# Kernel optimization log

Measured on AMD Instinct MI355X. Metric: run time of the kernel, lower is better.

The kernel has to match this reference:

```python
import jax, jax.numpy as jnp
import numpy as np

N = 100000
E = 1000000
IN_C, HID, OUT_C = 128, 128, 40
DROPOUT_P = 0.5
BN_EPS = 1e-5


def setup_inputs() -> dict:
    key = jax.random.key(0)
    ks = jax.random.split(key, 10)
    x = jax.random.normal(ks[0], (N, IN_C), dtype=jnp.float32)
    edge_index = jax.random.randint(ks[1], (2, E), 0, N, dtype=jnp.int32)

    def glorot(k, fan_in, fan_out):
        lim = np.sqrt(6.0 / (fan_in + fan_out)).astype(np.float32)
        return jax.random.uniform(k, (fan_in, fan_out), jnp.float32, -lim, lim)

    return {
        "x": x,
        "edge_index": edge_index,
        "W1": glorot(ks[2], IN_C, HID), "b1": jnp.zeros((HID,), jnp.float32),
        "g1": jnp.ones((HID,), jnp.float32), "be1": jnp.zeros((HID,), jnp.float32),
        "W2": glorot(ks[3], HID, HID), "b2": jnp.zeros((HID,), jnp.float32),
        "g2": jnp.ones((HID,), jnp.float32), "be2": jnp.zeros((HID,), jnp.float32),
        "W3": glorot(ks[4], HID, OUT_C), "b3": jnp.zeros((OUT_C,), jnp.float32),
    }


def _deg_inv_sqrt(dst):
    # degree from destination nodes, +1 for the added self loop (PyG gcn_norm)
    deg = jax.ops.segment_sum(jnp.ones((E,), jnp.float32), dst, num_segments=N) + 1.0
    return jax.lax.rsqrt(deg)


def _gcn_conv(h, W, b, src, dst, dinv):
    # h: [N, Cin] -> [N, Cout]; y = D^-1/2 (A + I) D^-1/2 (h W) + b
    hw = h @ W
    norm = dinv[src] * dinv[dst]                      # [E]
    msg = hw[src] * norm[:, None]                     # [E, Cout] gather (memory-bound)
    agg = jax.ops.segment_sum(msg, dst, num_segments=N)
    agg = agg + hw * (dinv * dinv)[:, None]           # self-loop contribution
    return agg + b


def _batchnorm(h, gamma, beta):
    mu = jnp.mean(h, axis=0)
    var = jnp.mean(jnp.square(h - mu), axis=0)        # biased, training mode
    return (h - mu) * jax.lax.rsqrt(var + BN_EPS) * gamma + beta


def _dropout(h, key):
    keep = jax.random.bernoulli(key, 1.0 - DROPOUT_P, h.shape)
    return jnp.where(keep, h / (1.0 - DROPOUT_P), 0.0)


def reference(x, edge_index, W1, b1, g1, be1, W2, b2, g2, be2, W3, b3):
    src, dst = edge_index[0], edge_index[1]
    dinv = _deg_inv_sqrt(dst)
    dk = jax.random.split(jax.random.key(42), 2)

    h = _gcn_conv(x, W1, b1, src, dst, dinv)
    h = _dropout(jax.nn.relu(_batchnorm(h, g1, be1)), dk[0])

    h = _gcn_conv(h, W2, b2, src, dst, dinv)
    h = _dropout(jax.nn.relu(_batchnorm(h, g2, be2)), dk[1])

    h = _gcn_conv(h, W3, b3, src, dst, dinv)
    return jax.nn.log_softmax(h, axis=1)
```

## Files before the change

### kernel.cpp

```cpp
#include <hip/hip_runtime.h>
#include <math.h>

typedef __attribute__((ext_vector_type(8))) short bf16x8;
typedef __attribute__((ext_vector_type(4))) float f32x4;

__device__ __forceinline__ float bfbits2f(unsigned short b){
  return __uint_as_float(((unsigned)b) << 16);
}
__device__ __forceinline__ unsigned short f2bfbits(float f){
  unsigned u = __float_as_uint(f);
  unsigned r = u + 0x7fffu + ((u >> 16) & 1u);
  return (unsigned short)(r >> 16);
}

__device__ __forceinline__ uint4 ld16(const void* __restrict__ base, unsigned byteoff){
  return *(const uint4*)((const char*)base + byteoff);
}
__device__ __forceinline__ uint2 ld8(const void* __restrict__ base, unsigned byteoff){
  return *(const uint2*)((const char*)base + byteoff);
}

__host__ __device__ __forceinline__ unsigned rotl32(unsigned v, int d){
  return (v << d) | (v >> (32 - d));
}
__host__ __device__ __forceinline__ void tf2x32(unsigned k0, unsigned k1,
                                                unsigned c0, unsigned c1,
                                                unsigned &o0, unsigned &o1)
{
  unsigned ks2 = k0 ^ k1 ^ 0x1BD11BDAu;
  unsigned x0 = c0 + k0, x1 = c1 + k1;
#define TFR(r) x0 += x1; x1 = rotl32(x1, r); x1 ^= x0;
  TFR(13) TFR(15) TFR(26) TFR(6)
  x0 += k1;  x1 += ks2 + 1u;
  TFR(17) TFR(29) TFR(16) TFR(24)
  x0 += ks2; x1 += k0 + 2u;
  TFR(13) TFR(15) TFR(26) TFR(6)
  x0 += k0;  x1 += k1 + 3u;
  TFR(17) TFR(29) TFR(16) TFR(24)
  x0 += k1;  x1 += ks2 + 4u;
  TFR(13) TFR(15) TFR(26) TFR(6)
  x0 += ks2; x1 += k0 + 5u;
#undef TFR
  o0 = x0; o1 = x1;
}

__global__ __launch_bounds__(256) void k_init(const float* __restrict__ W1,
                                              const float* __restrict__ W2,
                                              const float* __restrict__ W3,
                                              unsigned short* __restrict__ WT1,
                                              unsigned short* __restrict__ WT2,
                                              unsigned short* __restrict__ WT3,
                                              uint4* __restrict__ zbase, int zwords)
{
  if (blockIdx.x < 3){
    const float* W; unsigned short* WT; int Cout, Cpad;
    if (blockIdx.x == 0){ W = W1; WT = WT1; Cout = 128; Cpad = 128; }
    else if (blockIdx.x == 1){ W = W2; WT = WT2; Cout = 128; Cpad = 128; }
    else { W = W3; WT = WT3; Cout = 40; Cpad = 48; }
    int tot = Cpad * 128;
    for (int i = threadIdx.x; i < tot; i += 256){
      int n = i >> 7, k = i & 127;
      float v = (n < Cout) ? W[k * Cout + n] : 0.f;
      WT[i] = f2bfbits(v);
    }
  } else {
    int idx = (blockIdx.x - 3) * 256 + threadIdx.x;
    if (idx < zwords) zbase[idx] = make_uint4(0u, 0u, 0u, 0u);
  }
}

__global__ __launch_bounds__(256) void k_countpos(const int* __restrict__ dst,
                                                  int* __restrict__ cnt,
                                                  int* __restrict__ pos, int E)
{
  int g = blockIdx.x * 256 + threadIdx.x;
  int base = g * 4;
  if (base + 3 < E){
    int4 d = ((const int4*)dst)[g];
    int4 p;
    p.x = atomicAdd(&cnt[d.x], 1);
    p.y = atomicAdd(&cnt[d.y], 1);
    p.z = atomicAdd(&cnt[d.z], 1);
    p.w = atomicAdd(&cnt[d.w], 1);
    ((int4*)pos)[g] = p;
  } else {
    for (int j = 0; j < 4; j++){
      int e = base + j;
      if (e < E) pos[e] = atomicAdd(&cnt[dst[e]], 1);
    }
  }
}

__global__ __launch_bounds__(256) void k_blocksum(const int* __restrict__ cnt,
                                                  int* __restrict__ bsum, int N)
{
  __shared__ int sh[256];
  int t = threadIdx.x;
  int base = blockIdx.x * 1024 + t * 4;
  int s = 0;
  #pragma unroll
  for (int j = 0; j < 4; j++){ int i = base + j; if (i < N) s += cnt[i]; }
  sh[t] = s; __syncthreads();
  for (int off = 128; off; off >>= 1){
    if (t < off) sh[t] += sh[t + off];
    __syncthreads();
  }
  if (t == 0) bsum[blockIdx.x] = sh[0];
}

__global__ __launch_bounds__(256) void k_scanfinal(const int* __restrict__ cnt,
                                                   const int* __restrict__ bsum,
                                                   int* __restrict__ rowstart,
                                                   float* __restrict__ dinv,
                                                   int NB, int N)
{
  __shared__ int sh[256];
  int t = threadIdx.x;
  int vb = (t < NB) ? bsum[t] : 0;
  sh[t] = vb; __syncthreads();
  for (int off = 1; off < 256; off <<= 1){
    int x = sh[t];
    int y = (t >= off) ? sh[t - off] : 0;
    __syncthreads();
    sh[t] = x + y;
    __syncthreads();
  }
  if (blockIdx.x == 0 && t == 0) rowstart[N] = sh[NB - 1];
  int boffb = sh[blockIdx.x] - bsum[blockIdx.x];
  __syncthreads();
  int base = blockIdx.x * 1024 + t * 4;
  int c0 = 0, c1 = 0, c2 = 0, c3 = 0;
  if (base + 0 < N) c0 = cnt[base + 0];
  if (base + 1 < N) c1 = cnt[base + 1];
  if (base + 2 < N) c2 = cnt[base + 2];
  if (base + 3 < N) c3 = cnt[base + 3];
  int s = c0 + c1 + c2 + c3;
  sh[t] = s; __syncthreads();
  for (int off = 1; off < 256; off <<= 1){
    int x = sh[t];
    int y = (t >= off) ? sh[t - off] : 0;
    __syncthreads();
    sh[t] = x + y;
    __syncthreads();
  }
  int excl = sh[t] - s + boffb;
  if (base + 0 < N){ rowstart[base+0] = excl;          dinv[base+0] = rsqrtf((float)c0 + 1.f); }
  if (base + 1 < N){ rowstart[base+1] = excl+c0;       dinv[base+1] = rsqrtf((float)c1 + 1.f); }
  if (base + 2 < N){ rowstart[base+2] = excl+c0+c1;    dinv[base+2] = rsqrtf((float)c2 + 1.f); }
  if (base + 3 < N){ rowstart[base+3] = excl+c0+c1+c2; dinv[base+3] = rsqrtf((float)c3 + 1.f); }
}

__device__ __forceinline__ void fill_body(int bid,
                                          const int* __restrict__ src,
                                          const int* __restrict__ dst,
                                          const int* __restrict__ pos,
                                          const int* __restrict__ rowstart,
                                          int* __restrict__ csr, int E)
{
  int g = bid * 256 + threadIdx.x;
  int base = g * 4;
  if (base + 3 < E){
    int4 d = ((const int4*)dst)[g];
    int4 p = ((const int4*)pos)[g];
    int4 s = ((const int4*)src)[g];
    int r0 = rowstart[d.x], r1 = rowstart[d.y], r2 = rowstart[d.z], r3 = rowstart[d.w];
    csr[r0 + p.x] = s.x;
    csr[r1 + p.y] = s.y;
    csr[r2 + p.z] = s.z;
    csr[r3 + p.w] = s.w;
  } else {
    for (int j = 0; j < 4; j++){
      int e = base + j;
      if (e < E) csr[rowstart[dst[e]] + pos[e]] = src[e];
    }
  }
}

template<int NT, int MODE, int MASKGEN>
__device__ __forceinline__ void gemm_body(int bid,
                                          const void* __restrict__ Ap,
                                          const unsigned short* __restrict__ WT,
                                          const float* __restrict__ dinv,
                                          const float* __restrict__ stats,
                                          const float* __restrict__ g,
                                          const float* __restrict__ be,
                                          const unsigned* __restrict__ mask,
                                          unsigned* __restrict__ maskw,
                                          unsigned wk0, unsigned wk1, int Mw,
                                          float invN,
                                          unsigned short* __restrict__ outb,
                                          int N, int Cstride)
{
  __shared__ uint4 Wl4[NT * 16 * 16];
  __shared__ float bnS[128], bnB[128];
  const int t = threadIdx.x;
  const int w = t >> 6, l = t & 63;
  const int lm = l & 15, q = l >> 4;
  const long rb0 = (long)bid * 64;
  const int wrow0 = w * 16;
  const long grow = rb0 + wrow0 + lm;
  const bool inr = (grow < N);

  uint4 rawU[4];
  float4 rawF[4][2];
  uint4 mws;
  if (inr){
    #pragma unroll
    for (int kt = 0; kt < 4; kt++){
      int c = kt * 4 + q;
      if (MODE == 0){
        const float* ap = (const float*)Ap + grow * 128 + c * 8;
        rawF[kt][0] = *(const float4*)ap;
        rawF[kt][1] = *(const float4*)(ap + 4);
      } else {
        rawU[kt] = *(const uint4*)((const unsigned short*)Ap + grow * 128 + c * 8);
      }
    }
    if (MODE == 2) mws = *(const uint4*)(mask + ((unsigned)grow << 2));
  }

  {
    const uint4* s4 = (const uint4*)WT;
    const int tot = NT * 16 * 16;
    for (int i = t; i < tot; i += 256){
      int n = i >> 4, c = i & 15;
      Wl4[n * 16 + (c ^ (n & 15))] = s4[i];
    }
  }
  if (MODE == 2 && t < 128){
    float ss = 0.f, qq = 0.f;
    #pragma unroll
    for (int i = 0; i < 16; i++){
      ss += stats[i * 256 + t];
      qq += stats[i * 256 + 128 + t];
    }
    float mean = ss * invN;
    float var = fmaxf(qq * invN - mean * mean, 0.f);
    float rstd = rsqrtf(var + 1e-5f);
    float sc = g[t] * rstd;
    bnS[t] = sc * 2.f;
    bnB[t] = (be[t] - mean * sc) * 2.f;
  }
  __syncthreads();

  bf16x8 afr[4];
  #pragma unroll
  for (int kt = 0; kt < 4; kt++){
    uint4 chunk = make_uint4(0u, 0u, 0u, 0u);
    if (inr){
      if (MODE == 0){
        chunk.x = (unsigned)f2bfbits(rawF[kt][0].x) | ((unsigned)f2bfbits(rawF[kt][0].y) << 16);
        chunk.y = (unsigned)f2bfbits(rawF[kt][0].z) | ((unsigned)f2bfbits(rawF[kt][0].w) << 16);
        chunk.z = (unsigned)f2bfbits(rawF[kt][1].x) | ((unsigned)f2bfbits(rawF[kt][1].y) << 16);
        chunk.w = (unsigned)f2bfbits(rawF[kt][1].z) | ((unsigned)f2bfbits(rawF[kt][1].w) << 16);
      } else {
        int c = kt * 4 + q;
        unsigned mb = (&mws.x)[kt] >> (q * 8);
        const unsigned* rw = &rawU[kt].x;
        unsigned* cw = &chunk.x;
        #pragma unroll
        for (int h = 0; h < 4; h++){
          int ch = c * 8 + 2 * h;
          float f0 = bfbits2f((unsigned short)(rw[h] & 0xffffu));
          float f1 = bfbits2f((unsigned short)(rw[h] >> 16));
          f0 = fmaxf(fmaf(f0, bnS[ch],     bnB[ch]),     0.f);
          f1 = fmaxf(fmaf(f1, bnS[ch + 1], bnB[ch + 1]), 0.f);
          f0 = ((mb >> (2 * h))     & 1u) ? 0.f : f0;
          f1 = ((mb >> (2 * h + 1)) & 1u) ? 0.f : f1;
          cw[h] = (unsigned)f2bfbits(f0) | ((unsigned)f2bfbits(f1) << 16);
        }
      }
    }
    afr[kt] = *(bf16x8*)&chunk;
  }

  f32x4 acc[NT];
  #pragma unroll
  for (int nt = 0; nt < NT; nt++){
    acc[nt][0] = 0.f; acc[nt][1] = 0.f; acc[nt][2] = 0.f; acc[nt][3] = 0.f;
  }

  #pragma unroll
  for (int kt = 0; kt < 4; kt++){
    const int x = kt * 4 + q;
    #pragma unroll
    for (int nt = 0; nt < NT; nt++){
      int brow = nt * 16 + lm;
      bf16x8 wf = *(const bf16x8*)&Wl4[brow * 16 + (x ^ (brow & 15))];
      acc[nt] = __builtin_amdgcn_mfma_f32_16x16x32_bf16(wf, afr[kt], acc[nt], 0, 0, 0);
    }
  }

  if (inr){
    float dv = dinv[grow];
    char* rowp = (char*)outb + (size_t)grow * (unsigned)Cstride * 2u + (unsigned)(q * 4) * 2u;
    #pragma unroll
    for (int nt = 0; nt < NT; nt++){
      uint2 o;
      o.x = (unsigned)f2bfbits(acc[nt][0] * dv) | ((unsigned)f2bfbits(acc[nt][1] * dv) << 16);
      o.y = (unsigned)f2bfbits(acc[nt][2] * dv) | ((unsigned)f2bfbits(acc[nt][3] * dv) << 16);
      *(uint2*)(rowp + nt * 32) = o;
    }
  }

  if (MASKGEN){
    int gg = bid * 256 + t;
    if (gg < Mw){
      unsigned bits = 0u;
      #pragma unroll 4
      for (int j = 0; j < 32; j++){
        unsigned w0, w1;
        tf2x32(wk0, wk1, 0u, (unsigned)gg * 32u + (unsigned)j, w0, w1);
        bits |= (((w0 ^ w1) >> 31) << j);
      }
      maskw[gg] = bits;
    }
  }
}

__global__ __launch_bounds__(256) void k_g1f(const void* __restrict__ Ap,
                                             const unsigned short* __restrict__ WT,
                                             const float* __restrict__ dinv,
                                             unsigned* __restrict__ maskw,
                                             unsigned wk0, unsigned wk1, int Mw,
                                             unsigned short* __restrict__ outb, int N,
                                             const int* __restrict__ src,
                                             const int* __restrict__ dst,
                                             const int* __restrict__ pos,
                                             const int* __restrict__ rowstart,
                                             int* __restrict__ csr, int E, int gg)
{
  if ((int)blockIdx.x < gg){
    gemm_body<8, 0, 1>(blockIdx.x, Ap, WT, dinv, nullptr, nullptr, nullptr,
                       nullptr, maskw, wk0, wk1, Mw, 0.f, outb, N, 128);
  } else {
    fill_body(blockIdx.x - gg, src, dst, pos, rowstart, csr, E);
  }
}

template<int NT, int MODE, int MASKGEN>
__global__ __launch_bounds__(256) void k_gemm_mfma(const void* __restrict__ Ap,
                                                   const unsigned short* __restrict__ WT,
                                                   const float* __restrict__ dinv,
                                                   const float* __restrict__ stats,
                                                   const float* __restrict__ g,
                                                   const float* __restrict__ be,
                                                   const unsigned* __restrict__ mask,
                                                   unsigned* __restrict__ maskw,
                                                   unsigned wk0, unsigned wk1, int Mw,
                                                   float invN,
                                                   unsigned short* __restrict__ outb,
                                                   int N, int Cstride)
{
  gemm_body<NT, MODE, MASKGEN>(blockIdx.x, Ap, WT, dinv, stats, g, be, mask,
                               maskw, wk0, wk1, Mw, invN, outb, N, Cstride);
}

#define ACC8(U) do{ uint4 _u = (U); \
  a0 += __uint_as_float(_u.x << 16); \
  a1 += __uint_as_float(_u.x & 0xffff0000u); \
  a2 += __uint_as_float(_u.y << 16); \
  a3 += __uint_as_float(_u.y & 0xffff0000u); \
  a4 += __uint_as_float(_u.z << 16); \
  a5 += __uint_as_float(_u.z & 0xffff0000u); \
  a6 += __uint_as_float(_u.w << 16); \
  a7 += __uint_as_float(_u.w & 0xffff0000u); }while(0)

__global__ __launch_bounds__(256) void k_agg128s(const unsigned short* __restrict__ hw,
                                                 const int* __restrict__ rs,
                                                 const int* __restrict__ csr,
                                                 const float* __restrict__ dinv,
                                                 unsigned short* __restrict__ outb,
                                                 float* __restrict__ stats,
                                                 int N)
{
  const int l = threadIdx.x;
  const int ns = l >> 4;
  const int sl = l & 15;
  const int ty = threadIdx.y;
  const int grp = ty * 4 + ns;
  const int base = blockIdx.x * 32;
  const unsigned slB = (unsigned)sl * 16u;

  float s0=0.f,s1=0.f,s2=0.f,s3=0.f,s4=0.f,s5=0.f,s6=0.f,s7=0.f;
  float q0=0.f,q1=0.f,q2=0.f,q3=0.f,q4=0.f,q5=0.f,q6=0.f,q7=0.f;

  #pragma unroll 1
  for (int it = 0; it < 2; it++){
    int v = base + it * 16 + grp;
    if (v < N){
      float a0=0.f,a1=0.f,a2=0.f,a3=0.f,a4=0.f,a5=0.f,a6=0.f,a7=0.f;
      ACC8(ld16(hw, (unsigned)v * 256u + slB));
      int e0 = rs[v], e1 = rs[v + 1];
      int i = e0;
      for (; i + 4 <= e1; i += 4){
        int sa = csr[i], sb = csr[i+1], sc = csr[i+2], sd = csr[i+3];
        uint4 m0 = ld16(hw, (unsigned)sa * 256u + slB);
        uint4 m1 = ld16(hw, (unsigned)sb * 256u + slB);
        uint4 m2 = ld16(hw, (unsigned)sc * 256u + slB);
        uint4 m3 = ld16(hw, (unsigned)sd * 256u + slB);
        ACC8(m0); ACC8(m1); ACC8(m2); ACC8(m3);
      }
      for (; i < e1; i++){
        ACC8(ld16(hw, (unsigned)csr[i] * 256u + slB));
      }
      float dv = dinv[v];
      a0*=dv; a1*=dv; a2*=dv; a3*=dv; a4*=dv; a5*=dv; a6*=dv; a7*=dv;
      uint4 o;
      o.x = (unsigned)f2bfbits(a0) | ((unsigned)f2bfbits(a1) << 16);
      o.y = (unsigned)f2bfbits(a2) | ((unsigned)f2bfbits(a3) << 16);
      o.z = (unsigned)f2bfbits(a4) | ((unsigned)f2bfbits(a5) << 16);
      o.w = (unsigned)f2bfbits(a6) | ((unsigned)f2bfbits(a7) << 16);
      *(uint4*)((char*)outb + (unsigned)v * 256u + slB) = o;
      s0+=a0; q0=fmaf(a0,a0,q0);  s1+=a1; q1=fmaf(a1,a1,q1);
      s2+=a2; q2=fmaf(a2,a2,q2);  s3+=a3; q3=fmaf(a3,a3,q3);
      s4+=a4; q4=fmaf(a4,a4,q4);  s5+=a5; q5=fmaf(a5,a5,q5);
      s6+=a6; q6=fmaf(a6,a6,q6);  s7+=a7; q7=fmaf(a7,a7,q7);
    }
  }

  __shared__ float shS[16][128], shQ[16][128];
  *(float4*)&shS[grp][sl * 8]     = make_float4(s0, s1, s2, s3);
  *(float4*)&shS[grp][sl * 8 + 4] = make_float4(s4, s5, s6, s7);
  *(float4*)&shQ[grp][sl * 8]     = make_float4(q0, q1, q2, q3);
  *(float4*)&shQ[grp][sl * 8 + 4] = make_float4(q4, q5, q6, q7);
  __syncthreads();
  int t = ty * 64 + threadIdx.x;
  if (t < 128){
    float ss = 0.f, qq = 0.f;
    #pragma unroll
    for (int g2 = 0; g2 < 16; g2++){ ss += shS[g2][t]; qq += shQ[g2][t]; }
    float* dstat = stats + (blockIdx.x & 15) * 256;
    atomicAdd(&dstat[t], ss);
    atomicAdd(&dstat[128 + t], qq);
  }
}

__global__ __launch_bounds__(256) void k_agg40lsm(const unsigned short* __restrict__ hw,
                                                  const int* __restrict__ rs,
                                                  const int* __restrict__ csr,
                                                  const float* __restrict__ dinv,
                                                  const float* __restrict__ b3,
                                                  float* __restrict__ out, int N)
{
  const int l = threadIdx.x;
  const int ns = l >> 4, sl = l & 15;
  const int v = blockIdx.x * 16 + threadIdx.y * 4 + ns;
  const bool act = (v < N) && (sl < 10);
  const unsigned slB = (unsigned)sl * 8u;
  float a0 = 0.f, a1 = 0.f, a2 = 0.f, a3 = 0.f, dv = 1.f;
  if (act){
    dv = dinv[v];
    uint2 u = ld8(hw, (unsigned)v * 128u + slB);
    a0 = __uint_as_float(u.x << 16);
    a1 = __uint_as_float(u.x & 0xffff0000u);
    a2 = __uint_as_float(u.y << 16);
    a3 = __uint_as_float(u.y & 0xffff0000u);
    int e0 = rs[v], e1 = rs[v + 1];
    int i = e0;
#define ACCU2(U) do{ uint2 _u = (U); \
    a0 += __uint_as_float(_u.x << 16); \
    a1 += __uint_as_float(_u.x & 0xffff0000u); \
    a2 += __uint_as_float(_u.y << 16); \
    a3 += __uint_as_float(_u.y & 0xffff0000u); }while(0)
    for (; i + 4 <= e1; i += 4){
      int sa = csr[i], sb = csr[i+1], sc = csr[i+2], sd = csr[i+3];
      uint2 m0 = ld8(hw, (unsigned)sa * 128u + slB);
      uint2 m1 = ld8(hw, (unsigned)sb * 128u + slB);
      uint2 m2 = ld8(hw, (unsigned)sc * 128u + slB);
      uint2 m3 = ld8(hw, (unsigned)sd * 128u + slB);
      ACCU2(m0); ACCU2(m1); ACCU2(m2); ACCU2(m3);
    }
    for (; i < e1; i++){
      ACCU2(ld8(hw, (unsigned)csr[i] * 128u + slB));
    }
#undef ACCU2
  }
  float x0 = act ? fmaf(a0, dv, b3[sl * 4 + 0]) : -INFINITY;
  float x1 = act ? fmaf(a1, dv, b3[sl * 4 + 1]) : -INFINITY;
  float x2 = act ? fmaf(a2, dv, b3[sl * 4 + 2]) : -INFINITY;
  float x3 = act ? fmaf(a3, dv, b3[sl * 4 + 3]) : -INFINITY;
  float m = fmaxf(fmaxf(x0, x1), fmaxf(x2, x3));
  #pragma unroll
  for (int off = 8; off; off >>= 1) m = fmaxf(m, __shfl_xor(m, off, 16));
  float e = act ? (expf(x0 - m) + expf(x1 - m) + expf(x2 - m) + expf(x3 - m)) : 0.f;
  #pragma unroll
  for (int off = 8; off; off >>= 1) e += __shfl_xor(e, off, 16);
  float lse = m + logf(e);
  if (act){
    float4 o;
    o.x = x0 - lse; o.y = x1 - lse; o.z = x2 - lse; o.w = x3 - lse;
    *reinterpret_cast<float4*>(out + (size_t)v * 40 + sl * 4) = o;
  }
}

extern "C" void kernel_launch(void* const* d_in, const int* in_sizes, int n_in,
                              void* d_out, int out_size, void* d_ws, size_t ws_size,
                              hipStream_t stream)
{
  const float* x  = (const float*)d_in[0];
  const int* ei   = (const int*)d_in[1];
  const float* W1 = (const float*)d_in[2];
  const float* g1 = (const float*)d_in[4];
  const float* be1= (const float*)d_in[5];
  const float* W2 = (const float*)d_in[6];
  const float* g2 = (const float*)d_in[8];
  const float* be2= (const float*)d_in[9];
  const float* W3 = (const float*)d_in[10];
  const float* b3 = (const float*)d_in[11];
  float* out = (float*)d_out;

  const int N = in_sizes[0] / 128;
  const int E = in_sizes[1] / 2;
  const int* srcv = ei;
  const int* dstv = ei + E;

  char* ws = (char*)d_ws;
  size_t off = 0;
  auto take = [&](size_t bytes) -> void* {
    void* p = ws + off;
    off = (off + bytes + 255) & ~(size_t)255;
    return p;
  };
  int*   cnt      = (int*)  take((size_t)N * 4);
  float* stats1   = (float*)take(2 * 16 * 256 * 4);
  float* stats2   = stats1 + 16 * 256;
  size_t zlen = off;
  int*   pos      = (int*)  take((size_t)E * 4);
  int*   rowstart = (int*)  take((size_t)(N + 1) * 4);
  int*   csr      = (int*)  take((size_t)E * 4);
  float* dinv     = (float*)take((size_t)N * 4);
  int*   bsum     = (int*)  take(256 * 4);
  unsigned* mask1 = (unsigned*)take((size_t)N * 4 * 4);
  unsigned* mask2 = (unsigned*)take((size_t)N * 4 * 4);
  unsigned short* WT1 = (unsigned short*)take(128 * 128 * 2);
  unsigned short* WT2 = (unsigned short*)take(128 * 128 * 2);
  unsigned short* WT3 = (unsigned short*)take(48 * 128 * 2);
  unsigned short* bufX = (unsigned short*)take((size_t)N * 128 * 2);
  unsigned short* bufY = (unsigned short*)take((size_t)N * 128 * 2);
  (void)ws_size; (void)n_in; (void)out_size;

  unsigned l1k0, l1k1, l2k0, l2k1;
  tf2x32(0u, 42u, 0u, 0u, l1k0, l1k1);
  tf2x32(0u, 42u, 0u, 1u, l2k0, l2k1);

  const float invN = 1.0f / (float)N;
  const int M = N * 4;
  const int NB = (N + 1023) / 1024;
  dim3 wblk(64, 4);
  dim3 wgrid16((N + 15) / 16);
  dim3 wgrid32((N + 31) / 32);
  const int ggrid = (N + 63) / 64;
  const int egrid = (E + 1023) / 1024;
  const int zwords = (int)(zlen / 16);
  const int zgrid = 3 + (zwords + 255) / 256;

  k_init<<<zgrid, 256, 0, stream>>>(W1, W2, W3, WT1, WT2, WT3, (uint4*)cnt, zwords);
  k_countpos<<<egrid, 256, 0, stream>>>(dstv, cnt, pos, E);
  k_blocksum<<<NB, 256, 0, stream>>>(cnt, bsum, N);
  k_scanfinal<<<NB, 256, 0, stream>>>(cnt, bsum, rowstart, dinv, NB, N);

  k_g1f<<<ggrid + egrid, 256, 0, stream>>>(x, WT1, dinv, mask1, l1k0, l1k1, M,
      bufX, N, srcv, dstv, pos, rowstart, csr, E, ggrid);
  k_agg128s<<<wgrid32, wblk, 0, stream>>>(bufX, rowstart, csr, dinv, bufY, stats1, N);

  k_gemm_mfma<8, 2, 1><<<ggrid, 256, 0, stream>>>(bufY, WT2, dinv,
      stats1, g1, be1, mask1, mask2, l2k0, l2k1, M,
      invN, bufX, N, 128);
  k_agg128s<<<wgrid32, wblk, 0, stream>>>(bufX, rowstart, csr, dinv, bufY, stats2, N);

  k_gemm_mfma<3, 2, 0><<<ggrid, 256, 0, stream>>>(bufY, WT3, dinv,
      stats2, g2, be2, mask2, nullptr, 0u, 0u, 0,
      invN, bufX, N, 64);
  k_agg40lsm<<<wgrid16, wblk, 0, stream>>>(bufX, rowstart, csr, dinv, b3, out, N);
}
```

Measured before the change: 393.0 us.

## Fuse all stages into one persistent kernel with software grid barriers

Replaces the nine separate kernel launches with a single persistent kernel of 512 blocks that loops over virtual block indices for each stage and synchronises between stages with an atomic-counter grid barrier. Shared memory is unified into one buffer reused by every stage. The goal is to remove launch gaps and per-kernel tail effects. The cost is lower occupancy and parallelism per stage, since only 512 blocks of 256 threads run. Barrier spin overhead is added, and correctness depends on all 512 blocks being co-resident.

```diff
diff --git a/kernel.cpp b/kernel.cpp
--- a/kernel.cpp
+++ b/kernel.cpp
@@ -3,6 +3,8 @@
 
 typedef __attribute__((ext_vector_type(8))) short bf16x8;
 typedef __attribute__((ext_vector_type(4))) float f32x4;
+
+#define PB 512
 
 __device__ __forceinline__ float bfbits2f(unsigned short b){
   return __uint_as_float(((unsigned)b) << 16);
@@ -12,7 +14,6 @@
   unsigned r = u + 0x7fffu + ((u >> 16) & 1u);
   return (unsigned short)(r >> 16);
 }
-
 __device__ __forceinline__ uint4 ld16(const void* __restrict__ base, unsigned byteoff){
   return *(const uint4*)((const char*)base + byteoff);
 }
@@ -44,18 +45,40 @@
   o0 = x0; o1 = x1;
 }
 
-__global__ __launch_bounds__(256) void k_init(const float* __restrict__ W1,
-                                              const float* __restrict__ W2,
-                                              const float* __restrict__ W3,
-                                              unsigned short* __restrict__ WT1,
-                                              unsigned short* __restrict__ WT2,
-                                              unsigned short* __restrict__ WT3,
-                                              uint4* __restrict__ zbase, int zwords)
-{
-  if (blockIdx.x < 3){
+__device__ __forceinline__ void gsync(unsigned* __restrict__ bar){
+  __syncthreads();
+  if (threadIdx.x == 0){
+    __threadfence();
+    unsigned g = __hip_atomic_load(&bar[1], __ATOMIC_RELAXED, __HIP_MEMORY_SCOPE_AGENT);
+    unsigned a = __hip_atomic_fetch_add(&bar[0], 1u, __ATOMIC_ACQ_REL, __HIP_MEMORY_SCOPE_AGENT);
+    if (a == (unsigned)PB - 1u){
+      __hip_atomic_store(&bar[0], 0u, __ATOMIC_RELAXED, __HIP_MEMORY_SCOPE_AGENT);
+      __hip_atomic_fetch_add(&bar[1], 1u, __ATOMIC_ACQ_REL, __HIP_MEMORY_SCOPE_AGENT);
+    } else {
+      while (__hip_atomic_load(&bar[1], __ATOMIC_ACQUIRE, __HIP_MEMORY_SCOPE_AGENT) == g)
+        __builtin_amdgcn_s_sleep(2);
+    }
+    __threadfence();
+  }
+  __syncthreads();
+}
+
+#define SMEM_BYTES 33792
+
+
+__device__ __forceinline__ void init_body(int vb,
+                                          const float* __restrict__ W1,
+                                          const float* __restrict__ W2,
+                                          const float* __restrict__ W3,
+                                          unsigned short* __restrict__ WT1,
+                                          unsigned short* __restrict__ WT2,
+                                          unsigned short* __restrict__ WT3,
+                                          uint4* __restrict__ zbase, int zwords)
+{
+  if (vb < 3){
     const float* W; unsigned short* WT; int Cout, Cpad;
-    if (blockIdx.x == 0){ W = W1; WT = WT1; Cout = 128; Cpad = 128; }
-    else if (blockIdx.x == 1){ W = W2; WT = WT2; Cout = 128; Cpad = 128; }
+    if (vb == 0){ W = W1; WT = WT1; Cout = 128; Cpad = 128; }
+    else if (vb == 1){ W = W2; WT = WT2; Cout = 128; Cpad = 128; }
     else { W = W3; WT = WT3; Cout = 40; Cpad = 48; }
     int tot = Cpad * 128;
     for (int i = threadIdx.x; i < tot; i += 256){
@@ -64,16 +87,17 @@
       WT[i] = f2bfbits(v);
     }
   } else {
-    int idx = (blockIdx.x - 3) * 256 + threadIdx.x;
+    int idx = (vb - 3) * 256 + threadIdx.x;
     if (idx < zwords) zbase[idx] = make_uint4(0u, 0u, 0u, 0u);
   }
 }
 
-__global__ __launch_bounds__(256) void k_countpos(const int* __restrict__ dst,
-                                                  int* __restrict__ cnt,
-                                                  int* __restrict__ pos, int E)
-{
-  int g = blockIdx.x * 256 + threadIdx.x;
+__device__ __forceinline__ void countpos_body(int vb,
+                                              const int* __restrict__ dst,
+                                              int* __restrict__ cnt,
+                                              int* __restrict__ pos, int E)
+{
+  int g = vb * 256 + threadIdx.x;
   int base = g * 4;
   if (base + 3 < E){
     int4 d = ((const int4*)dst)[g];
@@ -91,12 +115,14 @@
   }
 }
 
-__global__ __launch_bounds__(256) void k_blocksum(const int* __restrict__ cnt,
-                                                  int* __restrict__ bsum, int N)
-{
-  __shared__ int sh[256];
+__device__ __forceinline__ void blocksum_body(int vb, char* smem,
+                                              const int* __restrict__ cnt,
+                                              int* __restrict__ bsum, int N)
+{
+  int* sh = (int*)smem;
+  __syncthreads();
   int t = threadIdx.x;
-  int base = blockIdx.x * 1024 + t * 4;
+  int base = vb * 1024 + t * 4;
   int s = 0;
   #pragma unroll
   for (int j = 0; j < 4; j++){ int i = base + j; if (i < N) s += cnt[i]; }
@@ -105,19 +131,21 @@
     if (t < off) sh[t] += sh[t + off];
     __syncthreads();
   }
-  if (t == 0) bsum[blockIdx.x] = sh[0];
-}
-
-__global__ __launch_bounds__(256) void k_scanfinal(const int* __restrict__ cnt,
-                                                   const int* __restrict__ bsum,
-                                                   int* __restrict__ rowstart,
-                                                   float* __restrict__ dinv,
-                                                   int NB, int N)
-{
-  __shared__ int sh[256];
+  if (t == 0) bsum[vb] = sh[0];
+}
+
+__device__ __forceinline__ void scanfinal_body(int vb, char* smem,
+                                               const int* __restrict__ cnt,
+                                               const int* __restrict__ bsum,
+                                               int* __restrict__ rowstart,
+                                               float* __restrict__ dinv,
+                                               int NB, int N)
+{
+  int* sh = (int*)smem;
+  __syncthreads();
   int t = threadIdx.x;
-  int vb = (t < NB) ? bsum[t] : 0;
-  sh[t] = vb; __syncthreads();
+  int vb2 = (t < NB) ? bsum[t] : 0;
+  sh[t] = vb2; __syncthreads();
   for (int off = 1; off < 256; off <<= 1){
     int x = sh[t];
     int y = (t >= off) ? sh[t - off] : 0;
@@ -125,10 +153,10 @@
     sh[t] = x + y;
     __syncthreads();
   }
-  if (blockIdx.x == 0 && t == 0) rowstart[N] = sh[NB - 1];
-  int boffb = sh[blockIdx.x] - bsum[blockIdx.x];
-  __syncthreads();
-  int base = blockIdx.x * 1024 + t * 4;
+  if (vb == 0 && t == 0) rowstart[N] = sh[NB - 1];
+  int boffb = sh[vb] - bsum[vb];
+  __syncthreads();
+  int base = vb * 1024 + t * 4;
   int c0 = 0, c1 = 0, c2 = 0, c3 = 0;
   if (base + 0 < N) c0 = cnt[base + 0];
   if (base + 1 < N) c1 = cnt[base + 1];
@@ -177,7 +205,7 @@
 }
 
 template<int NT, int MODE, int MASKGEN>
-__device__ __forceinline__ void gemm_body(int bid,
+__device__ __forceinline__ void gemm_body(int bid, char* smem,
                                           const void* __restrict__ Ap,
                                           const unsigned short* __restrict__ WT,
                                           const float* __restrict__ dinv,
@@ -191,8 +219,10 @@
                                           unsigned short* __restrict__ outb,
                                           int N, int Cstride)
 {
-  __shared__ uint4 Wl4[NT * 16 * 16];
-  __shared__ float bnS[128], bnB[128];
+  uint4* Wl4 = (uint4*)smem;
+  float* bnS = (float*)(smem + NT * 4096);
+  float* bnB = bnS + 128;
+  __syncthreads();
   const int t = threadIdx.x;
   const int w = t >> 6, l = t & 63;
   const int lm = l & 15, q = l >> 4;
@@ -318,44 +348,6 @@
   }
 }
 
-__global__ __launch_bounds__(256) void k_g1f(const void* __restrict__ Ap,
-                                             const unsigned short* __restrict__ WT,
-                                             const float* __restrict__ dinv,
-                                             unsigned* __restrict__ maskw,
-                                             unsigned wk0, unsigned wk1, int Mw,
-                                             unsigned short* __restrict__ outb, int N,
-                                             const int* __restrict__ src,
-                                             const int* __restrict__ dst,
-                                             const int* __restrict__ pos,
-                                             const int* __restrict__ rowstart,
-                                             int* __restrict__ csr, int E, int gg)
-{
-  if ((int)blockIdx.x < gg){
-    gemm_body<8, 0, 1>(blockIdx.x, Ap, WT, dinv, nullptr, nullptr, nullptr,
-                       nullptr, maskw, wk0, wk1, Mw, 0.f, outb, N, 128);
-  } else {
-    fill_body(blockIdx.x - gg, src, dst, pos, rowstart, csr, E);
-  }
-}
-
-template<int NT, int MODE, int MASKGEN>
-__global__ __launch_bounds__(256) void k_gemm_mfma(const void* __restrict__ Ap,
-                                                   const unsigned short* __restrict__ WT,
-                                                   const float* __restrict__ dinv,
-                                                   const float* __restrict__ stats,
-                                                   const float* __restrict__ g,
-                                                   const float* __restrict__ be,
-                                                   const unsigned* __restrict__ mask,
-                                                   unsigned* __restrict__ maskw,
-                                                   unsigned wk0, unsigned wk1, int Mw,
-                                                   float invN,
-                                                   unsigned short* __restrict__ outb,
-                                                   int N, int Cstride)
-{
-  gemm_body<NT, MODE, MASKGEN>(blockIdx.x, Ap, WT, dinv, stats, g, be, mask,
-                               maskw, wk0, wk1, Mw, invN, outb, N, Cstride);
-}
-
 #define ACC8(U) do{ uint4 _u = (U); \
   a0 += __uint_as_float(_u.x << 16); \
   a1 += __uint_as_float(_u.x & 0xffff0000u); \
@@ -366,20 +358,25 @@
   a6 += __uint_as_float(_u.w << 16); \
   a7 += __uint_as_float(_u.w & 0xffff0000u); }while(0)
 
-__global__ __launch_bounds__(256) void k_agg128s(const unsigned short* __restrict__ hw,
-                                                 const int* __restrict__ rs,
-                                                 const int* __restrict__ csr,
-                                                 const float* __restrict__ dinv,
-                                                 unsigned short* __restrict__ outb,
-                                                 float* __restrict__ stats,
-                                                 int N)
-{
-  const int l = threadIdx.x;
+__device__ __forceinline__ void agg128_body(int vb, char* smem,
+                                            const unsigned short* __restrict__ hw,
+                                            const int* __restrict__ rs,
+                                            const int* __restrict__ csr,
+                                            const float* __restrict__ dinv,
+                                            unsigned short* __restrict__ outb,
+                                            float* __restrict__ stats,
+                                            int N)
+{
+  float (*shS)[128] = (float(*)[128])smem;
+  float (*shQ)[128] = (float(*)[128])(smem + 8192);
+  __syncthreads();
+  const int tt = threadIdx.x;
+  const int l = tt & 63;
+  const int ty = tt >> 6;
   const int ns = l >> 4;
   const int sl = l & 15;
-  const int ty = threadIdx.y;
   const int grp = ty * 4 + ns;
-  const int base = blockIdx.x * 32;
+  const int base = vb * 32;
   const unsigned slB = (unsigned)sl * 16u;
 
   float s0=0.f,s1=0.f,s2=0.f,s3=0.f,s4=0.f,s5=0.f,s6=0.f,s7=0.f;
@@ -419,33 +416,34 @@
     }
   }
 
-  __shared__ float shS[16][128], shQ[16][128];
   *(float4*)&shS[grp][sl * 8]     = make_float4(s0, s1, s2, s3);
   *(float4*)&shS[grp][sl * 8 + 4] = make_float4(s4, s5, s6, s7);
   *(float4*)&shQ[grp][sl * 8]     = make_float4(q0, q1, q2, q3);
   *(float4*)&shQ[grp][sl * 8 + 4] = make_float4(q4, q5, q6, q7);
   __syncthreads();
-  int t = ty * 64 + threadIdx.x;
-  if (t < 128){
+  if (tt < 128){
     float ss = 0.f, qq = 0.f;
     #pragma unroll
-    for (int g2 = 0; g2 < 16; g2++){ ss += shS[g2][t]; qq += shQ[g2][t]; }
-    float* dstat = stats + (blockIdx.x & 15) * 256;
-    atomicAdd(&dstat[t], ss);
-    atomicAdd(&dstat[128 + t], qq);
-  }
-}
-
-__global__ __launch_bounds__(256) void k_agg40lsm(const unsigned short* __restrict__ hw,
-                                                  const int* __restrict__ rs,
-                                                  const int* __restrict__ csr,
-                                                  const float* __restrict__ dinv,
-                                                  const float* __restrict__ b3,
-                                                  float* __restrict__ out, int N)
-{
-  const int l = threadIdx.x;
+    for (int g2 = 0; g2 < 16; g2++){ ss += shS[g2][tt]; qq += shQ[g2][tt]; }
+    float* dstat = stats + (vb & 15) * 256;
+    atomicAdd(&dstat[tt], ss);
+    atomicAdd(&dstat[128 + tt], qq);
+  }
+}
+
+__device__ __forceinline__ void agg40_body(int vb,
+                                           const unsigned short* __restrict__ hw,
+                                           const int* __restrict__ rs,
+                                           const int* __restrict__ csr,
+                                           const float* __restrict__ dinv,
+                                           const float* __restrict__ b3,
+                                           float* __restrict__ out, int N)
+{
+  const int tt = threadIdx.x;
+  const int l = tt & 63;
+  const int ty = tt >> 6;
   const int ns = l >> 4, sl = l & 15;
-  const int v = blockIdx.x * 16 + threadIdx.y * 4 + ns;
+  const int v = vb * 16 + ty * 4 + ns;
   const bool act = (v < N) && (sl < 10);
   const unsigned slB = (unsigned)sl * 8u;
   float a0 = 0.f, a1 = 0.f, a2 = 0.f, a3 = 0.f, dv = 1.f;
@@ -494,6 +492,73 @@
   }
 }
 
+__global__ __launch_bounds__(256, 4) void k_mega(
+    const float* __restrict__ x, const int* __restrict__ srcv,
+    const int* __restrict__ dstv,
+    const float* __restrict__ W1, const float* __restrict__ W2,
+    const float* __restrict__ W3,
+    const float* __restrict__ g1, const float* __restrict__ be1,
+    const float* __restrict__ g2, const float* __restrict__ be2,
+    const float* __restrict__ b3,
+    unsigned* __restrict__ bar,
+    int* __restrict__ cnt, float* __restrict__ stats1, float* __restrict__ stats2,
+    int* __restrict__ pos, int* __restrict__ rowstart, int* __restrict__ csr,
+    float* __restrict__ dinv, int* __restrict__ bsum,
+    unsigned* __restrict__ mask1, unsigned* __restrict__ mask2,
+    unsigned short* __restrict__ WT1, unsigned short* __restrict__ WT2,
+    unsigned short* __restrict__ WT3,
+    unsigned short* __restrict__ bufX, unsigned short* __restrict__ bufY,
+    float* __restrict__ out,
+    unsigned l1k0, unsigned l1k1, unsigned l2k0, unsigned l2k1,
+    float invN, int M, int zwords, int N, int E)
+{
+  __shared__ __align__(16) char smem[SMEM_BYTES];
+  const int bx = blockIdx.x;
+  const int eg = (E + 1023) / 1024;
+  const int NB = (N + 1023) / 1024;
+  const int gg = (N + 63) / 64;
+  const int wg32 = (N + 31) / 32;
+  const int wg16 = (N + 15) / 16;
+  const int zg = 3 + (zwords + 255) / 256;
+
+  for (int vb = bx; vb < zg; vb += PB)
+    init_body(vb, W1, W2, W3, WT1, WT2, WT3, (uint4*)cnt, zwords);
+  gsync(bar);
+  for (int vb = bx; vb < eg; vb += PB)
+    countpos_body(vb, dstv, cnt, pos, E);
+  gsync(bar);
+  for (int vb = bx; vb < NB; vb += PB)
+    blocksum_body(vb, smem, cnt, bsum, N);
+  gsync(bar);
+  for (int vb = bx; vb < NB; vb += PB)
+    scanfinal_body(vb, smem, cnt, bsum, rowstart, dinv, NB, N);
+  gsync(bar);
+  for (int vb = bx; vb < gg + eg; vb += PB){
+    if (vb < gg)
+      gemm_body<8, 0, 1>(vb, smem, x, WT1, dinv, nullptr, nullptr, nullptr,
+                         nullptr, mask1, l1k0, l1k1, M, 0.f, bufX, N, 128);
+    else
+      fill_body(vb - gg, srcv, dstv, pos, rowstart, csr, E);
+  }
+  gsync(bar);
+  for (int vb = bx; vb < wg32; vb += PB)
+    agg128_body(vb, smem, bufX, rowstart, csr, dinv, bufY, stats1, N);
+  gsync(bar);
+  for (int vb = bx; vb < gg; vb += PB)
+    gemm_body<8, 2, 1>(vb, smem, bufY, WT2, dinv, stats1, g1, be1,
+                       mask1, mask2, l2k0, l2k1, M, invN, bufX, N, 128);
+  gsync(bar);
+  for (int vb = bx; vb < wg32; vb += PB)
+    agg128_body(vb, smem, bufX, rowstart, csr, dinv, bufY, stats2, N);
+  gsync(bar);
+  for (int vb = bx; vb < gg; vb += PB)
+    gemm_body<3, 2, 0>(vb, smem, bufY, WT3, dinv, stats2, g2, be2,
+                       mask2, nullptr, 0u, 0u, 0, invN, bufX, N, 64);
+  gsync(bar);
+  for (int vb = bx; vb < wg16; vb += PB)
+    agg40_body(vb, bufX, rowstart, csr, dinv, b3, out, N);
+}
+
 extern "C" void kernel_launch(void* const* d_in, const int* in_sizes, int n_in,
                               void* d_out, int out_size, void* d_ws, size_t ws_size,
                               hipStream_t stream)
@@ -522,10 +587,12 @@
     off = (off + bytes + 255) & ~(size_t)255;
     return p;
   };
+  unsigned* bar   = (unsigned*)take(2 * 4);
+  size_t zstart = off;
   int*   cnt      = (int*)  take((size_t)N * 4);
   float* stats1   = (float*)take(2 * 16 * 256 * 4);
   float* stats2   = stats1 + 16 * 256;
-  size_t zlen = off;
+  size_t zlen = off - zstart;
   int*   pos      = (int*)  take((size_t)E * 4);
   int*   rowstart = (int*)  take((size_t)(N + 1) * 4);
   int*   csr      = (int*)  take((size_t)E * 4);
@@ -546,31 +613,12 @@
 
   const float invN = 1.0f / (float)N;
   const int M = N * 4;
-  const int NB = (N + 1023) / 1024;
-  dim3 wblk(64, 4);
-  dim3 wgrid16((N + 15) / 16);
-  dim3 wgrid32((N + 31) / 32);
-  const int ggrid = (N + 63) / 64;
-  const int egrid = (E + 1023) / 1024;
   const int zwords = (int)(zlen / 16);
-  const int zgrid = 3 + (zwords + 255) / 256;
-
-  k_init<<<zgrid, 256, 0, stream>>>(W1, W2, W3, WT1, WT2, WT3, (uint4*)cnt, zwords);
-  k_countpos<<<egrid, 256, 0, stream>>>(dstv, cnt, pos, E);
-  k_blocksum<<<NB, 256, 0, stream>>>(cnt, bsum, N);
-  k_scanfinal<<<NB, 256, 0, stream>>>(cnt, bsum, rowstart, dinv, NB, N);
-
-  k_g1f<<<ggrid + egrid, 256, 0, stream>>>(x, WT1, dinv, mask1, l1k0, l1k1, M,
-      bufX, N, srcv, dstv, pos, rowstart, csr, E, ggrid);
-  k_agg128s<<<wgrid32, wblk, 0, stream>>>(bufX, rowstart, csr, dinv, bufY, stats1, N);
-
-  k_gemm_mfma<8, 2, 1><<<ggrid, 256, 0, stream>>>(bufY, WT2, dinv,
-      stats1, g1, be1, mask1, mask2, l2k0, l2k1, M,
-      invN, bufX, N, 128);
-  k_agg128s<<<wgrid32, wblk, 0, stream>>>(bufX, rowstart, csr, dinv, bufY, stats2, N);
-
-  k_gemm_mfma<3, 2, 0><<<ggrid, 256, 0, stream>>>(bufY, WT3, dinv,
-      stats2, g2, be2, mask2, nullptr, 0u, 0u, 0,
-      invN, bufX, N, 64);
-  k_agg40lsm<<<wgrid16, wblk, 0, stream>>>(bufX, rowstart, csr, dinv, b3, out, N);
-}
+
+  hipMemsetAsync(bar, 0, 2 * 4, stream);
+  k_mega<<<PB, 256, 0, stream>>>(x, srcv, dstv, W1, W2, W3,
+      g1, be1, g2, be2, b3, bar,
+      cnt, stats1, stats2, pos, rowstart, csr, dinv, bsum,
+      mask1, mask2, WT1, WT2, WT3, bufX, bufY, out,
+      l1k0, l1k1, l2k0, l2k1, invN, M, zwords, N, E);
+}
```

Measured after the change: 1.524 ms. 288% more time.
